# Optimization experiments

Hardware: AMD Instinct MI355X
Metric: run time of the kernel (lower is better)

The kernel has to match this reference:

```python
import jax, jax.numpy as jnp
import numpy as np

SPARSE_COMPRESSION_RATIO = 0.5  # config.sparse_compression_ratio


def setup_inputs() -> dict:
    key = jax.random.key(0)
    kv_cache = jax.random.normal(key, (2, 32, 4096, 128), dtype=jnp.float32)
    return {"kv_cache": kv_cache}


def reference(kv_cache):
    # elements_to_keep = int(numel * (1 - ratio))
    total = kv_cache.size
    k = int(total * (1.0 - SPARSE_COMPRESSION_RATIO))
    flat = kv_cache.reshape(-1)
    # torch.topk(|x|, k, largest=True) -> indices of k largest magnitudes
    _, top_idx = jax.lax.top_k(jnp.abs(flat), k)
    # scatter mask, then elementwise multiply (zeros out non-top-k entries)
    mask = jnp.zeros((total,), dtype=jnp.bool_).at[top_idx].set(True)
    return kv_cache * mask.reshape(kv_cache.shape)
```

## Files before the change

### kernel.cpp

```cpp
#include <hip/hip_runtime.h>
#include <stdint.h>
#include <math.h>


#define NTHR 256
#define MASK31 0x7fffffffu

typedef unsigned int v4u __attribute__((ext_vector_type(4)));

#define SH_OFF    0
#define SH_BINS   8192
#define CH_OFF    8192
#define CH_BINS   4096
#define SCL_OFF   12288
#define ZERO_WORDS 12320
#define HIC_OFF   12320
#define PCN_OFF   16416
#define OVFP_OFF  20512
#define OVFP_CAP  16384
#define CMP_OFF   53536
#define CMP_CAP   4096
#define PAIRS_OFF 131072
#define SEG_CAP   1024
#define NBLK_MAIN 4096
#define STG_CAP   1024

__global__ void zero_ws_kernel(uint32_t* __restrict__ ws) {
    int i = blockIdx.x * blockDim.x + threadIdx.x;
    if (i < ZERO_WORDS) ws[i] = 0;
}

__global__ void sample_bracket_kernel(const v4u* __restrict__ xv, long long n4,
                                      uint32_t* __restrict__ ws,
                                      uint32_t ksmM, uint32_t kspM) {
    __shared__ uint32_t lh[SH_BINS];
    __shared__ uint32_t csum[NTHR];
    __shared__ uint32_t cpre[NTHR];
    __shared__ int sBHi, sB1, amLast;
    for (int i = threadIdx.x; i < SH_BINS; i += NTHR) lh[i] = 0;
    __syncthreads();
    long long S4 = n4 >> 5;
    long long T = (long long)gridDim.x * NTHR;
    for (long long s = (long long)blockIdx.x * NTHR + threadIdx.x; s < S4; s += T) {
        long long idx4 = ((s >> 9) << 14) | (s & 511);
        if (idx4 < n4) {
            v4u v = xv[idx4];
            atomicAdd(&lh[(v.x & MASK31) >> 18], 1u);
            atomicAdd(&lh[(v.y & MASK31) >> 18], 1u);
            atomicAdd(&lh[(v.z & MASK31) >> 18], 1u);
            atomicAdd(&lh[(v.w & MASK31) >> 18], 1u);
        }
    }
    __syncthreads();
    for (int i = threadIdx.x; i < SH_BINS; i += NTHR)
        if (lh[i]) atomicAdd(&ws[SH_OFF + i], lh[i]);
    __syncthreads();
    if (threadIdx.x == 0) {
        uint32_t old = atomicAdd(&ws[SCL_OFF + 7], 1u);
        amLast = (old == gridDim.x - 1u) ? 1 : 0;
        sBHi = -1; sB1 = -1;
    }
    __syncthreads();
    if (!amLast) return;
    for (int i = threadIdx.x; i < SH_BINS; i += NTHR)
        lh[i] = atomicAdd(&ws[SH_OFF + i], 0u);
    __syncthreads();
    uint32_t s = 0;
    for (int i = 0; i < 32; ++i) s += lh[threadIdx.x * 32 + i];
    csum[threadIdx.x] = s;
    __syncthreads();
    if (threadIdx.x == 0) {
        uint32_t run = 0;
        for (int c = NTHR - 1; c >= 0; --c) { cpre[c] = run; run += csum[c]; }
    }
    __syncthreads();
    {
        int c = threadIdx.x;
        int hitHi = -1, hitB1 = -1;
        uint32_t excl = cpre[c];
        for (int bb = c * 32 + 31; bb >= c * 32; --bb) {
            uint32_t cnt = lh[bb];
            uint32_t incl = excl + cnt;
            if (hitHi < 0 && incl >= ksmM) hitHi = bb;
            if (hitB1 < 0 && excl >= kspM) hitB1 = bb;
            excl = incl;
        }
        if (hitHi >= 0) atomicMax(&sBHi, hitHi);
        if (hitB1 >= 0) atomicMax(&sB1, hitB1);
    }
    __syncthreads();
    if (threadIdx.x == 0) {
        int bHi = sBHi < 0 ? 0 : sBHi;
        int bLo = sB1 + 1;
        if (bLo > bHi) bLo = bHi;
        if (bLo < 0) bLo = 0;
        int sbins = bHi - bLo + 1;
        int clog = 0; while ((1 << clog) < sbins) ++clog;
        int spanBits = 18 + clog;
        int shift1 = spanBits - 12;
        if (shift1 < 0) shift1 = 0;
        ws[SCL_OFF + 0] = ((uint32_t)bLo) << 18;
        ws[SCL_OFF + 1] = ((uint32_t)(bHi + 1)) << 18;
        ws[SCL_OFF + 2] = (uint32_t)shift1;
    }
}

__global__ void fused_main_kernel(const uint32_t* __restrict__ x,
                                  uint32_t* __restrict__ out, long long n,
                                  uint32_t* __restrict__ ws) {
    __shared__ uint2 stage[STG_CAP];
    __shared__ uint32_t cnt, redHi[NTHR / 64];
    const uint32_t uLo = ws[SCL_OFF + 0];
    const uint32_t uHi = ws[SCL_OFF + 1];
    const uint32_t span = uHi - uLo;
    if (threadIdx.x == 0) cnt = 0u;
    __syncthreads();

    const v4u* __restrict__ xv = (const v4u*)x;
    v4u* __restrict__ ov = (v4u*)out;
    long long n4 = n >> 2;
    const long long stride = (long long)gridDim.x * NTHR;
    const long long i0 = (long long)blockIdx.x * NTHR + threadIdx.x;

    uint32_t myHi = 0;
    uint32_t myCnt = 0;
    uint32_t s0v = 0, s0i = 0, s1v = 0, s1i = 0;
    uint32_t s2v = 0, s2i = 0, s3v = 0, s3i = 0;

    for (long long i = i0; i < n4; i += stride) {
        v4u v = xv[i];
        uint32_t c0 = v.x & MASK31, c1 = v.y & MASK31;
        uint32_t c2 = v.z & MASK31, c3 = v.w & MASK31;
        myHi += (uint32_t)(c0 >= uHi) + (uint32_t)(c1 >= uHi)
              + (uint32_t)(c2 >= uHi) + (uint32_t)(c3 >= uHi);
        v4u o;
        o.x = (c0 >= uHi) ? v.x : 0u;
        o.y = (c1 >= uHi) ? v.y : 0u;
        o.z = (c2 >= uHi) ? v.z : 0u;
        o.w = (c3 >= uHi) ? v.w : 0u;
        uint32_t h0 = (c0 - uLo) < span ? 1u : 0u;
        uint32_t h1 = (c1 - uLo) < span ? 1u : 0u;
        uint32_t h2 = (c2 - uLo) < span ? 1u : 0u;
        uint32_t h3 = (c3 - uLo) < span ? 1u : 0u;
        if (h0 | h1 | h2 | h3) {
            uint32_t e0 = (uint32_t)(i << 2);
#define CAPT(hx, val, eidx) if (hx) { \
    if (myCnt == 0)      { s0v = (val); s0i = (eidx); } \
    else if (myCnt == 1) { s1v = (val); s1i = (eidx); } \
    else if (myCnt == 2) { s2v = (val); s2i = (eidx); } \
    else if (myCnt == 3) { s3v = (val); s3i = (eidx); } \
    ++myCnt; }
            CAPT(h0, v.x, e0 + 0u)
            CAPT(h1, v.y, e0 + 1u)
            CAPT(h2, v.z, e0 + 2u)
            CAPT(h3, v.w, e0 + 3u)
#undef CAPT
        }
        ov[i] = o;
    }

    uint2* __restrict__ ovfp = (uint2*)(ws + OVFP_OFF);
#define PUSHP(val, eidx) { \
    uint32_t p_ = atomicAdd(&cnt, 1u); \
    uint2 pr_ = make_uint2((val), (eidx)); \
    if (p_ < STG_CAP) stage[p_] = pr_; \
    else { uint32_t g_ = atomicAdd(&ws[SCL_OFF + 5], 1u); \
           if (g_ < OVFP_CAP) ovfp[g_] = pr_; } }

    if (blockIdx.x == 0) {
        for (long long idx = (n4 << 2) + threadIdx.x; idx < n; idx += NTHR) {
            uint32_t v = x[idx];
            uint32_t u = v & MASK31;
            myHi += (uint32_t)(u >= uHi);
            if (u - uLo < span) PUSHP(v, (uint32_t)idx)
            out[idx] = (u >= uHi) ? v : 0u;
        }
    }

    if (myCnt <= 4u) {
        if (myCnt > 0u) PUSHP(s0v, s0i)
        if (myCnt > 1u) PUSHP(s1v, s1i)
        if (myCnt > 2u) PUSHP(s2v, s2i)
        if (myCnt > 3u) PUSHP(s3v, s3i)
    } else {
        for (long long i = i0; i < n4; i += stride) {
            v4u v = xv[i];
            uint32_t e0 = (uint32_t)(i << 2);
            uint32_t u;
            u = v.x & MASK31; if (u - uLo < span) PUSHP(v.x, e0 + 0u)
            u = v.y & MASK31; if (u - uLo < span) PUSHP(v.y, e0 + 1u)
            u = v.z & MASK31; if (u - uLo < span) PUSHP(v.z, e0 + 2u)
            u = v.w & MASK31; if (u - uLo < span) PUSHP(v.w, e0 + 3u)
        }
    }
#undef PUSHP

    for (int o = 32; o > 0; o >>= 1) myHi += __shfl_down(myHi, o);
    if ((threadIdx.x & 63) == 0) redHi[threadIdx.x >> 6] = myHi;
    __syncthreads();
    if (threadIdx.x == 0) {
        uint32_t tot = 0;
        for (int w = 0; w < NTHR / 64; ++w) tot += redHi[w];
        ws[HIC_OFF + blockIdx.x] = tot;
        uint32_t c = cnt < STG_CAP ? cnt : STG_CAP;
        cnt = c;
        ws[PCN_OFF + blockIdx.x] = c;
    }
    __syncthreads();
    uint2* __restrict__ seg = (uint2*)(ws + PAIRS_OFF) + (size_t)blockIdx.x * SEG_CAP;
    uint32_t c = cnt;
    for (uint32_t q = threadIdx.x; q < c; q += NTHR) seg[q] = stage[q];
}

__global__ void cand_hist_sel_kernel(uint32_t* __restrict__ ws, uint32_t k) {
    __shared__ uint32_t lh[CH_BINS];
    __shared__ uint32_t csum[NTHR];
    __shared__ uint32_t cpre[NTHR];
    __shared__ int amLast;
    __shared__ uint32_t sBase2, sRem2;
    uint32_t uLo = ws[SCL_OFF + 0], shift1 = ws[SCL_OFF + 2];
    for (int i = threadIdx.x; i < CH_BINS; i += NTHR) lh[i] = 0;
    __syncthreads();
    const uint2* pairs = (const uint2*)(ws + PAIRS_OFF);
    for (int g = 0; g < NBLK_MAIN / 256; ++g) {
        uint32_t sidx = blockIdx.x + (uint32_t)g * 256u;
        uint32_t c = ws[PCN_OFF + sidx];
        const uint2* seg = pairs + (size_t)sidx * SEG_CAP;
        for (uint32_t i = threadIdx.x; i < c; i += NTHR) {
            uint32_t u = seg[i].x & MASK31;
            atomicAdd(&lh[((u - uLo) >> shift1) & (CH_BINS - 1)], 1u);
        }
    }
    if (blockIdx.x == 0) {
        uint32_t c = ws[SCL_OFF + 5]; if (c > OVFP_CAP) c = OVFP_CAP;
        const uint2* ovfp = (const uint2*)(ws + OVFP_OFF);
        for (uint32_t i = threadIdx.x; i < c; i += NTHR) {
            uint32_t u = ovfp[i].x & MASK31;
            atomicAdd(&lh[((u - uLo) >> shift1) & (CH_BINS - 1)], 1u);
        }
    }
    __syncthreads();
    for (int i = threadIdx.x; i < CH_BINS; i += NTHR)
        if (lh[i]) atomicAdd(&ws[CH_OFF + i], lh[i]);
    __syncthreads();
    if (threadIdx.x == 0) {
        uint32_t old = atomicAdd(&ws[SCL_OFF + 8], 1u);
        amLast = (old == gridDim.x - 1u) ? 1 : 0;
    }
    __syncthreads();
    if (!amLast) return;
    for (int i = threadIdx.x; i < CH_BINS; i += NTHR)
        lh[i] = atomicAdd(&ws[CH_OFF + i], 0u);
    uint32_t part = 0;
    for (int i = threadIdx.x; i < NBLK_MAIN; i += NTHR) part += ws[HIC_OFF + i];
    for (int o = 32; o > 0; o >>= 1) part += __shfl_down(part, o);
    csum[threadIdx.x] = 0;
    __syncthreads();
    if ((threadIdx.x & 63) == 0) csum[threadIdx.x >> 6] = part;
    __syncthreads();
    uint32_t cntHi = csum[0] + csum[1] + csum[2] + csum[3];
    __syncthreads();
    uint32_t s = 0;
    for (int i = 0; i < 16; ++i) s += lh[threadIdx.x * 16 + i];
    csum[threadIdx.x] = s;
    __syncthreads();
    __shared__ uint32_t sKp;
    if (threadIdx.x == 0) {
        uint32_t run = 0;
        for (int c = NTHR - 1; c >= 0; --c) { cpre[c] = run; run += csum[c]; }
        uint32_t total = cpre[0] + csum[0];
        uint32_t kp = (k > cntHi) ? (k - cntHi) : 1u;
        if (kp > total) kp = total;
        if (kp < 1u) kp = 1u;
        sKp = kp;
        sBase2 = uLo; sRem2 = 1u;
    }
    __syncthreads();
    uint32_t kp = sKp;
    if (cpre[threadIdx.x] < kp && kp <= cpre[threadIdx.x] + csum[threadIdx.x]) {
        uint32_t excl = cpre[threadIdx.x];
        for (int bb = threadIdx.x * 16 + 15; bb >= threadIdx.x * 16; --bb) {
            uint32_t cnt = lh[bb];
            if (excl + cnt >= kp) {
                sBase2 = uLo + (((uint32_t)bb) << shift1);
                sRem2 = kp - excl;
                break;
            }
            excl += cnt;
        }
    }
    __syncthreads();
    if (threadIdx.x == 0) { ws[SCL_OFF + 3] = sBase2; ws[SCL_OFF + 4] = sRem2; }
}

__global__ void gather_fixup_kernel(uint32_t* __restrict__ ws,
                                    uint32_t* __restrict__ out) {
    __shared__ uint2 l3s[CMP_CAP];
    __shared__ int amLast;
    uint32_t base2 = ws[SCL_OFF + 3], rem2 = ws[SCL_OFF + 4];
    uint32_t width = 1u << ws[SCL_OFF + 2];
    uint32_t tHi2 = base2 + width;
    const uint2* pairs = (const uint2*)(ws + PAIRS_OFF);
    uint32_t* cmp = ws + CMP_OFF;

#define PROC(pr) { \
    uint32_t u_ = (pr).x & MASK31; \
    if (u_ >= tHi2) { out[(pr).y] = (pr).x; } \
    else if (u_ - base2 < width) { \
        uint32_t p_ = atomicAdd(&ws[SCL_OFF + 9], 1u); \
        if (p_ < CMP_CAP) { \
            atomicExch(&cmp[2 * p_], (pr).x); \
            atomicExch(&cmp[2 * p_ + 1], (pr).y); } } }

    for (int g = 0; g < NBLK_MAIN / 256; ++g) {
        uint32_t sidx = blockIdx.x + (uint32_t)g * 256u;
        uint32_t c = ws[PCN_OFF + sidx];
        const uint2* seg = pairs + (size_t)sidx * SEG_CAP;
        for (uint32_t i = threadIdx.x; i < c; i += NTHR) {
            uint2 pr = seg[i];
            PROC(pr)
        }
    }
    if (blockIdx.x == 0) {
        uint32_t c = ws[SCL_OFF + 5]; if (c > OVFP_CAP) c = OVFP_CAP;
        const uint2* ovfp = (const uint2*)(ws + OVFP_OFF);
        for (uint32_t i = threadIdx.x; i < c; i += NTHR) {
            uint2 pr = ovfp[i];
            PROC(pr)
        }
    }
#undef PROC
    __syncthreads();
    if (threadIdx.x == 0) {
        uint32_t old = atomicAdd(&ws[SCL_OFF + 10], 1u);
        amLast = (old == gridDim.x - 1u) ? 1 : 0;
    }
    __syncthreads();
    if (!amLast) return;
    uint32_t c3 = atomicAdd(&ws[SCL_OFF + 9], 0u);
    if (c3 > CMP_CAP) c3 = CMP_CAP;
    for (uint32_t i = threadIdx.x; i < c3; i += NTHR) {
        uint2 pr;
        pr.x = atomicAdd(&cmp[2 * i], 0u);
        pr.y = atomicAdd(&cmp[2 * i + 1], 0u);
        l3s[i] = pr;
    }
    __syncthreads();
    for (uint32_t i = threadIdx.x; i < c3; i += NTHR) {
        uint2 me = l3s[i];
        uint32_t u = me.x & MASK31;
        uint32_t rank = 0;
        for (uint32_t p = 0; p < c3; ++p) {
            uint2 q2 = l3s[p];
            uint32_t up = q2.x & MASK31;
            rank += (up > u || (up == u && q2.y < me.y)) ? 1u : 0u;
        }
        if (rank < rem2) out[me.y] = me.x;
    }
}

extern "C" void kernel_launch(void* const* d_in, const int* in_sizes, int n_in,
                              void* d_out, int out_size, void* d_ws, size_t ws_size,
                              hipStream_t stream) {
    const uint32_t* x = (const uint32_t*)d_in[0];
    uint32_t* out = (uint32_t*)d_out;
    uint32_t* ws = (uint32_t*)d_ws;
    long long n = (long long)in_sizes[0];

    const double ratio = 0.5;
    long long k = (long long)((double)n * (1.0 - ratio));
    if (k < 1) k = 1;
    if (k > n) k = n;

    long long n4 = n >> 2;
    long long S = (n4 >> 5) << 2;
    if (S < 4) S = (n4 << 2);
    long long ks = (long long)((double)k * ((double)S / (double)n));
    long long M = (long long)(9.0 * sqrt((double)S * 0.25)) + 64;
    uint32_t ksmM = (uint32_t)((ks - M) < 1 ? 1 : (ks - M));
    uint32_t kspM = (uint32_t)((ks + M) > S ? S : (ks + M));

    zero_ws_kernel<<<(ZERO_WORDS + NTHR - 1) / NTHR, NTHR, 0, stream>>>(ws);
    sample_bracket_kernel<<<256, NTHR, 0, stream>>>((const v4u*)x, n4, ws, ksmM, kspM);
    fused_main_kernel<<<NBLK_MAIN, NTHR, 0, stream>>>(x, out, n, ws);
    cand_hist_sel_kernel<<<256, NTHR, 0, stream>>>(ws, (uint32_t)k);
    gather_fixup_kernel<<<256, NTHR, 0, stream>>>(ws, out);
}
```

Measured before the change: 134.1 us.

## Merge histogram-select and gather-fixup into one cooperative kernel with grid sync

Combines the candidate histogram/threshold selection kernel and the gather/fixup kernel into a single cooperative launch. Grid-wide syncs replace the last-block-done atomic counters, so every block computes the threshold redundantly instead of one block writing it to global memory. The goal is to drop one kernel launch and the serial tail of a last-block section. In exchange it adds cooperative-launch overhead and grid-barrier cost, and the histogram and compaction buffers now share one block of shared memory.

```diff
diff --git a/kernel.cpp b/kernel.cpp
--- a/kernel.cpp
+++ b/kernel.cpp
@@ -1,6 +1,9 @@
 #include <hip/hip_runtime.h>
+#include <hip/hip_cooperative_groups.h>
 #include <stdint.h>
 #include <math.h>
+
+namespace cg = cooperative_groups;
 
 
 #define NTHR 256
@@ -212,16 +215,20 @@
     for (uint32_t q = threadIdx.x; q < c; q += NTHR) seg[q] = stage[q];
 }
 
-__global__ void cand_hist_sel_kernel(uint32_t* __restrict__ ws, uint32_t k) {
-    __shared__ uint32_t lh[CH_BINS];
+__global__ void refine_kernel(uint32_t* __restrict__ ws, uint32_t k,
+                              uint32_t* __restrict__ out) {
+    __shared__ uint32_t smem[2 * CMP_CAP];
     __shared__ uint32_t csum[NTHR];
     __shared__ uint32_t cpre[NTHR];
-    __shared__ int amLast;
-    __shared__ uint32_t sBase2, sRem2;
-    uint32_t uLo = ws[SCL_OFF + 0], shift1 = ws[SCL_OFF + 2];
+    __shared__ uint32_t sBase2, sRem2, sKp;
+    uint32_t* lh = smem;
+    uint2* l3s = (uint2*)smem;
+    const uint32_t uLo = ws[SCL_OFF + 0], shift1 = ws[SCL_OFF + 2];
+    const uint2* pairs = (const uint2*)(ws + PAIRS_OFF);
+    uint32_t* cmp = ws + CMP_OFF;
+
     for (int i = threadIdx.x; i < CH_BINS; i += NTHR) lh[i] = 0;
     __syncthreads();
-    const uint2* pairs = (const uint2*)(ws + PAIRS_OFF);
     for (int g = 0; g < NBLK_MAIN / 256; ++g) {
         uint32_t sidx = blockIdx.x + (uint32_t)g * 256u;
         uint32_t c = ws[PCN_OFF + sidx];
@@ -242,13 +249,9 @@
     __syncthreads();
     for (int i = threadIdx.x; i < CH_BINS; i += NTHR)
         if (lh[i]) atomicAdd(&ws[CH_OFF + i], lh[i]);
-    __syncthreads();
-    if (threadIdx.x == 0) {
-        uint32_t old = atomicAdd(&ws[SCL_OFF + 8], 1u);
-        amLast = (old == gridDim.x - 1u) ? 1 : 0;
-    }
-    __syncthreads();
-    if (!amLast) return;
+
+    cg::this_grid().sync();
+
     for (int i = threadIdx.x; i < CH_BINS; i += NTHR)
         lh[i] = atomicAdd(&ws[CH_OFF + i], 0u);
     uint32_t part = 0;
@@ -264,7 +267,6 @@
     for (int i = 0; i < 16; ++i) s += lh[threadIdx.x * 16 + i];
     csum[threadIdx.x] = s;
     __syncthreads();
-    __shared__ uint32_t sKp;
     if (threadIdx.x == 0) {
         uint32_t run = 0;
         for (int c = NTHR - 1; c >= 0; --c) { cpre[c] = run; run += csum[c]; }
@@ -290,18 +292,9 @@
         }
     }
     __syncthreads();
-    if (threadIdx.x == 0) { ws[SCL_OFF + 3] = sBase2; ws[SCL_OFF + 4] = sRem2; }
-}
-
-__global__ void gather_fixup_kernel(uint32_t* __restrict__ ws,
-                                    uint32_t* __restrict__ out) {
-    __shared__ uint2 l3s[CMP_CAP];
-    __shared__ int amLast;
-    uint32_t base2 = ws[SCL_OFF + 3], rem2 = ws[SCL_OFF + 4];
-    uint32_t width = 1u << ws[SCL_OFF + 2];
-    uint32_t tHi2 = base2 + width;
-    const uint2* pairs = (const uint2*)(ws + PAIRS_OFF);
-    uint32_t* cmp = ws + CMP_OFF;
+    const uint32_t base2 = sBase2, rem2 = sRem2;
+    const uint32_t width = 1u << shift1;
+    const uint32_t tHi2 = base2 + width;
 
 #define PROC(pr) { \
     uint32_t u_ = (pr).x & MASK31; \
@@ -311,7 +304,6 @@
         if (p_ < CMP_CAP) { \
             atomicExch(&cmp[2 * p_], (pr).x); \
             atomicExch(&cmp[2 * p_ + 1], (pr).y); } } }
-
     for (int g = 0; g < NBLK_MAIN / 256; ++g) {
         uint32_t sidx = blockIdx.x + (uint32_t)g * 256u;
         uint32_t c = ws[PCN_OFF + sidx];
@@ -330,13 +322,10 @@
         }
     }
 #undef PROC
-    __syncthreads();
-    if (threadIdx.x == 0) {
-        uint32_t old = atomicAdd(&ws[SCL_OFF + 10], 1u);
-        amLast = (old == gridDim.x - 1u) ? 1 : 0;
-    }
-    __syncthreads();
-    if (!amLast) return;
+
+    cg::this_grid().sync();
+
+    if (blockIdx.x != 0) return;
     uint32_t c3 = atomicAdd(&ws[SCL_OFF + 9], 0u);
     if (c3 > CMP_CAP) c3 = CMP_CAP;
     for (uint32_t i = threadIdx.x; i < c3; i += NTHR) {
@@ -383,6 +372,9 @@
     zero_ws_kernel<<<(ZERO_WORDS + NTHR - 1) / NTHR, NTHR, 0, stream>>>(ws);
     sample_bracket_kernel<<<256, NTHR, 0, stream>>>((const v4u*)x, n4, ws, ksmM, kspM);
     fused_main_kernel<<<NBLK_MAIN, NTHR, 0, stream>>>(x, out, n, ws);
-    cand_hist_sel_kernel<<<256, NTHR, 0, stream>>>(ws, (uint32_t)k);
-    gather_fixup_kernel<<<256, NTHR, 0, stream>>>(ws, out);
-}
+
+    uint32_t k32 = (uint32_t)k;
+    void* args[] = { (void*)&ws, (void*)&k32, (void*)&out };
+    hipLaunchCooperativeKernel((const void*)refine_kernel, dim3(256), dim3(NTHR),
+                               args, 0, stream);
+}
```

Result: slower. 193.4 us (+44.2%).
